# Optimization experiments

Hardware: AMD Instinct MI355X
Metric: run time of the kernel (lower is better)

Reference implementation:

```python
import jax, jax.numpy as jnp
import numpy as np

N_ITERS = 5
STRICT_MAXIMA_BONUS = 10.0
MAX_SUBPIXEL_SHIFT = 0.6
DILATION_RADIUS = 1
EPS = 1e-7


def _dense_solve(x):
    """Per-voxel 3x3x3 quadratic-fit solve (Cramer's rule) on interior voxels.

    Returns full-size (zero-padded) sx, sy, ss, g.s, solved arrays.
    Axis convention: s = depth/scale (D), y = height (H), x = width (W).
    """
    c  = x[:, :, 1:-1, 1:-1, 1:-1]
    xp = x[:, :, 1:-1, 1:-1, 2:];   xm = x[:, :, 1:-1, 1:-1, :-2]
    yp = x[:, :, 1:-1, 2:, 1:-1];   ym = x[:, :, 1:-1, :-2, 1:-1]
    sp = x[:, :, 2:, 1:-1, 1:-1];   sm = x[:, :, :-2, 1:-1, 1:-1]
    xpyp = x[:, :, 1:-1, 2:, 2:];   xmyp = x[:, :, 1:-1, 2:, :-2]
    xpym = x[:, :, 1:-1, :-2, 2:];  xmym = x[:, :, 1:-1, :-2, :-2]
    xpsp = x[:, :, 2:, 1:-1, 2:];   xmsp = x[:, :, 2:, 1:-1, :-2]
    xpsm = x[:, :, :-2, 1:-1, 2:];  xmsm = x[:, :, :-2, 1:-1, :-2]
    ypsp = x[:, :, 2:, 2:, 1:-1];   ymsp = x[:, :, 2:, :-2, 1:-1]
    ypsm = x[:, :, :-2, 2:, 1:-1];  ymsm = x[:, :, :-2, :-2, 1:-1]
    gx = 0.5 * (xp - xm)
    gy = 0.5 * (yp - ym)
    gs = 0.5 * (sp - sm)
    dxx = xp - 2.0 * c + xm
    dyy = yp - 2.0 * c + ym
    dss = sp - 2.0 * c + sm
    dxy = 0.25 * (xpyp - xmyp - xpym + xmym)
    dxs = 0.25 * (xpsp - xmsp - xpsm + xmsm)
    dys = 0.25 * (ypsp - ymsp - ypsm + ymsm)
    cf00 = dyy * dss - dys * dys
    cf01 = dxy * dss - dys * dxs
    cf02 = dxy * dys - dyy * dxs
    det = dxx * cf00 - dxy * cf01 + dxs * cf02
    solved = jnp.abs(det) > EPS
    safe_det = jnp.where(solved, det, jnp.ones_like(det))
    r0, r1, r2 = -gx, -gy, -gs
    sx = (r0 * cf00 - dxy * (r1 * dss - dys * r2) + dxs * (r1 * dys - dyy * r2)) / safe_det
    sy = (dxx * (r1 * dss - dys * r2) - r0 * cf01 + dxs * (dxy * r2 - r1 * dxs)) / safe_det
    ss = (dxx * (dyy * r2 - r1 * dys) - dxy * (dxy * r2 - r1 * dxs) + r0 * cf02) / safe_det
    gds = gx * sx + gy * sy + gs * ss
    pad = ((0, 0), (0, 0), (1, 1), (1, 1), (1, 1))
    return (jnp.pad(sx, pad), jnp.pad(sy, pad), jnp.pad(ss, pad),
            jnp.pad(gds, pad), jnp.pad(solved, pad))


def reference(input, nms_mask):
    x = input
    B, C, D, H, W = x.shape
    dt = x.dtype
    HW = H * W
    DHW = D * HW
    r = DILATION_RADIUS

    sx_f, sy_f, ss_f, gds_f, sol_f = _dense_solve(x)
    sx_f = sx_f.reshape(-1); sy_f = sy_f.reshape(-1); ss_f = ss_f.reshape(-1)
    gds_f = gds_f.reshape(-1); sol_f = sol_f.reshape(-1)
    xf = x.reshape(-1)

    dg = jnp.arange(D, dtype=jnp.int32)[:, None, None]
    hg = jnp.arange(H, dtype=jnp.int32)[None, :, None]
    wg = jnp.arange(W, dtype=jnp.int32)[None, None, :]
    bcg = (jnp.arange(B * C, dtype=jnp.int32) * DHW).reshape(B, C, 1, 1, 1)

    zi = jnp.zeros((B, C, D, H, W), jnp.int32)
    dd, dh, dw = zi, zi, zi              # integer centre offsets (s, y, x)
    valid = nms_mask                      # only NMS maxima are tracked
    zf = jnp.zeros((B, C, D, H, W), dt)
    shift_x, shift_y, shift_s, gds_k = zf, zf, zf, zf

    for _ in range(N_ITERS):
        di = jnp.clip(dg + dd, 1, D - 2)
        hi = jnp.clip(hg + dh, 1, H - 2)
        wi = jnp.clip(wg + dw, 1, W - 2)
        flat = bcg + di * HW + hi * W + wi
        sx = sx_f[flat]; sy = sy_f[flat]; ss = ss_f[flat]
        gds = gds_f[flat]; sol = sol_f[flat]
        valid = valid & sol
        vf = valid.astype(dt)
        shift_x = sx * vf
        shift_y = sy * vf
        shift_s = ss * vf
        gds_k = gds * vf
        step_x = (jnp.sign(shift_x) * (jnp.abs(shift_x) > MAX_SUBPIXEL_SHIFT)).astype(jnp.int32)
        step_y = (jnp.sign(shift_y) * (jnp.abs(shift_y) > MAX_SUBPIXEL_SHIFT)).astype(jnp.int32)
        step_s = (jnp.sign(shift_s) * (jnp.abs(shift_s) > MAX_SUBPIXEL_SHIFT)).astype(jnp.int32)
        dw = dw + step_x; dh = dh + step_y; dd = dd + step_s
        # moving outside the dilated precompute region invalidates the keypoint
        valid = valid & (jnp.abs(dd) <= r) & (jnp.abs(dh) <= r) & (jnp.abs(dw) <= r)

    di = jnp.clip(dg + dd, 1, D - 2)
    hi = jnp.clip(hg + dh, 1, H - 2)
    wi = jnp.clip(wg + dw, 1, W - 2)
    flat = bcg + di * HW + hi * W + wi
    cur_val = xf[flat]

    refined = jnp.where(valid, cur_val + 0.5 * gds_k, x)
    y_max = jnp.where(nms_mask, refined + STRICT_MAXIMA_BONUS, x)

    fd = dg.astype(dt); fh = hg.astype(dt); fw = wg.astype(dt)
    cs = jnp.where(valid, (dg + dd).astype(dt) + shift_s, jnp.broadcast_to(fd, x.shape))
    cx = jnp.where(valid, (wg + dw).astype(dt) + shift_x, jnp.broadcast_to(fw, x.shape))
    cy = jnp.where(valid, (hg + dh).astype(dt) + shift_y, jnp.broadcast_to(fh, x.shape))
    coords_max = jnp.stack([cs, cx, cy], axis=2)  # (B,C,3,D,H,W): [scale, x, y]
    return coords_max, y_max


def setup_inputs() -> dict:
    key = jax.random.key(0)
    k1, k2 = jax.random.split(key)
    B, C, D, H, W = 2, 4, 6, 512, 512
    x = jax.random.normal(k1, (B, C, D, H, W), dtype=jnp.float32)
    m = jax.random.uniform(k2, (B, C, D, H, W)) < 0.001
    interior = jnp.zeros((B, C, D, H, W), dtype=bool).at[:, :, 1:-1, 1:-1, 1:-1].set(True)
    return {"input": x, "nms_mask": m & interior}
```

## Files before the change

### kernel.cpp

```cpp
#include <hip/hip_runtime.h>

#pragma clang fp contract(off)

constexpr int B_ = 2, C_ = 4, D_ = 6, H_ = 512, W_ = 512;
constexpr int HW_  = H_ * W_;
constexpr int DHW_ = D_ * HW_;
constexpr int BC_  = B_ * C_;
constexpr int TOT_ = BC_ * DHW_;

#define EPS_ 1e-7f
#define MAX_SHIFT_ 0.6f
#define BONUS_ 10.0f
#define N_ITERS_ 5

typedef float f32x4 __attribute__((ext_vector_type(4)));
typedef int   i32x4 __attribute__((ext_vector_type(4)));

__device__ __forceinline__ void solve3(const float* __restrict__ p,
                                       float& sx, float& sy, float& ss,
                                       float& gds, bool& sol)
{
    #pragma clang fp contract(off)
    float c    = p[0];
    float xp   = p[1],          xm   = p[-1];
    float yp   = p[W_],         ym   = p[-W_];
    float spv  = p[HW_],        smv  = p[-HW_];
    float xpyp = p[W_ + 1],     xmyp = p[W_ - 1];
    float xpym = p[-W_ + 1],    xmym = p[-W_ - 1];
    float xpsp = p[HW_ + 1],    xmsp = p[HW_ - 1];
    float xpsm = p[-HW_ + 1],   xmsm = p[-HW_ - 1];
    float ypsp = p[HW_ + W_],   ymsp = p[HW_ - W_];
    float ypsm = p[-HW_ + W_],  ymsm = p[-HW_ - W_];

    float gx = 0.5f * (xp - xm);
    float gy = 0.5f * (yp - ym);
    float gs = 0.5f * (spv - smv);
    float dxx = xp - 2.0f * c + xm;
    float dyy = yp - 2.0f * c + ym;
    float dss = spv - 2.0f * c + smv;
    float dxy = 0.25f * (xpyp - xmyp - xpym + xmym);
    float dxs = 0.25f * (xpsp - xmsp - xpsm + xmsm);
    float dys = 0.25f * (ypsp - ymsp - ypsm + ymsm);

    float cf00 = dyy * dss - dys * dys;
    float cf01 = dxy * dss - dys * dxs;
    float cf02 = dxy * dys - dyy * dxs;
    float det  = dxx * cf00 - dxy * cf01 + dxs * cf02;
    sol = fabsf(det) > EPS_;
    float sd = sol ? det : 1.0f;
    float r0 = -gx, r1 = -gy, r2 = -gs;
    sx = (r0 * cf00 - dxy * (r1 * dss - dys * r2) + dxs * (r1 * dys - dyy * r2)) / sd;
    sy = (dxx * (r1 * dss - dys * r2) - r0 * cf01 + dxs * (dxy * r2 - r1 * dxs)) / sd;
    ss = (dxx * (dyy * r2 - r1 * dys) - dxy * (dxy * r2 - r1 * dxs) + r0 * cf02) / sd;
    gds = gx * sx + gy * sy + gs * ss;
}

__global__ __launch_bounds__(256)
void AdaptiveQuadInterp3d_kernel(const float* __restrict__ x,
                                 const int* __restrict__ mask,
                                 float* __restrict__ out)
{
    int tid = blockIdx.x * 256 + threadIdx.x;
    int e   = tid * 4;

    int w0 = e & (W_ - 1);
    int h  = (e >> 9) & (H_ - 1);
    int t  = e >> 18;
    int d  = t % D_;
    int bc = t / D_;
    int sp = e - bc * DHW_;

    const f32x4 xv = *reinterpret_cast<const f32x4*>(x + e);
    const i32x4 mv = *reinterpret_cast<const i32x4*>(mask + e);

    float fd = (float)d, fh = (float)h;
    float cs0 = fd, cs1 = fd, cs2 = fd, cs3 = fd;
    float cx0 = (float)w0,       cx1 = (float)(w0 + 1);
    float cx2 = (float)(w0 + 2), cx3 = (float)(w0 + 3);
    float cy0 = fh, cy1 = fh, cy2 = fh, cy3 = fh;
    float y0 = xv.x, y1 = xv.y, y2 = xv.z, y3 = xv.w;

    int anym = mv.x | mv.y | mv.z | mv.w;

    if (__ballot(anym != 0) != 0ULL) {
        if (anym != 0) {
            const float* xb = x + bc * DHW_;

            auto walk = [&](int mj, int w, float xc,
                            float& cs, float& cx, float& cy, float& yy) {
                #pragma clang fp contract(off)
                if (mj == 0) return;
                int dsd = 0, dsh = 0, dsw = 0;
                bool valid = true;
                float shx = 0.0f, shy = 0.0f, shs = 0.0f, gk = 0.0f;

                #pragma unroll 1
                for (int it = 0; it < N_ITERS_; ++it) {
                    int di = min(max(d + dsd, 1), D_ - 2);
                    int hi = min(max(h + dsh, 1), H_ - 2);
                    int wi = min(max(w + dsw, 1), W_ - 2);
                    const float* p = xb + di * HW_ + hi * W_ + wi;

                    float sx, sy, ssv, gds; bool sol;
                    solve3(p, sx, sy, ssv, gds, sol);

                    if (!sol) { valid = false; break; }

                    shx = sx; shy = sy; shs = ssv; gk = gds;

                    int stx = (shx > MAX_SHIFT_) ? 1 : ((shx < -MAX_SHIFT_) ? -1 : 0);
                    int sty = (shy > MAX_SHIFT_) ? 1 : ((shy < -MAX_SHIFT_) ? -1 : 0);
                    int sts = (shs > MAX_SHIFT_) ? 1 : ((shs < -MAX_SHIFT_) ? -1 : 0);
                    dsw += stx;
                    dsh += sty;
                    dsd += sts;
                    valid = (abs(dsd) <= 1) && (abs(dsh) <= 1) && (abs(dsw) <= 1);
                    if (!valid) break;
                    if ((stx | sty | sts) == 0) break;
                }

                if (valid) {
                    int di = min(max(d + dsd, 1), D_ - 2);
                    int hi = min(max(h + dsh, 1), H_ - 2);
                    int wi = min(max(w + dsw, 1), W_ - 2);
                    float cur = xb[di * HW_ + hi * W_ + wi];
                    cs = (float)(d + dsd) + shs;
                    cx = (float)(w + dsw) + shx;
                    cy = (float)(h + dsh) + shy;
                    yy = (cur + 0.5f * gk) + BONUS_;
                } else {
                    yy = xc + BONUS_;
                }
            };

            walk(mv.x, w0 + 0, xv.x, cs0, cx0, cy0, y0);
            walk(mv.y, w0 + 1, xv.y, cs1, cx1, cy1, y1);
            walk(mv.z, w0 + 2, xv.z, cs2, cx2, cy2, y2);
            walk(mv.w, w0 + 3, xv.w, cs3, cx3, cy3, y3);
        }
    }

    f32x4 csv = { cs0, cs1, cs2, cs3 };
    f32x4 cxv = { cx0, cx1, cx2, cx3 };
    f32x4 cyv = { cy0, cy1, cy2, cy3 };
    f32x4 yv  = { y0,  y1,  y2,  y3  };

    float* cb = out + (bc * 3) * DHW_ + sp;
    __builtin_nontemporal_store(csv, reinterpret_cast<f32x4*>(cb));
    __builtin_nontemporal_store(cxv, reinterpret_cast<f32x4*>(cb + DHW_));
    __builtin_nontemporal_store(cyv, reinterpret_cast<f32x4*>(cb + 2 * DHW_));
    __builtin_nontemporal_store(yv,
        reinterpret_cast<f32x4*>(out + BC_ * 3 * DHW_ + e));
}

extern "C" void kernel_launch(void* const* d_in, const int* in_sizes, int n_in,
                              void* d_out, int out_size, void* d_ws, size_t ws_size,
                              hipStream_t stream) {
    const float* x    = (const float*)d_in[0];
    const int*   mask = (const int*)d_in[1];
    float*       out  = (float*)d_out;

    int blocks = TOT_ / (256 * 4);
    AdaptiveQuadInterp3d_kernel<<<blocks, 256, 0, stream>>>(x, mask, out);
}
```

Before: 275.0 us.

## Process eight elements per thread and store defaults before sparse refinement

```diff
diff --git a/kernel.cpp b/kernel.cpp
--- a/kernel.cpp
+++ b/kernel.cpp
@@ -61,7 +61,7 @@
                                  float* __restrict__ out)
 {
     int tid = blockIdx.x * 256 + threadIdx.x;
-    int e   = tid * 4;
+    int e   = tid * 8;
 
     int w0 = e & (W_ - 1);
     int h  = (e >> 9) & (H_ - 1);
@@ -70,26 +70,41 @@
     int bc = t / D_;
     int sp = e - bc * DHW_;
 
-    const f32x4 xv = *reinterpret_cast<const f32x4*>(x + e);
-    const i32x4 mv = *reinterpret_cast<const i32x4*>(mask + e);
+    const f32x4 xa = *reinterpret_cast<const f32x4*>(x + e);
+    const f32x4 xbv = *reinterpret_cast<const f32x4*>(x + e + 4);
+    const i32x4 ma = *reinterpret_cast<const i32x4*>(mask + e);
+    const i32x4 mb = *reinterpret_cast<const i32x4*>(mask + e + 4);
 
     float fd = (float)d, fh = (float)h;
-    float cs0 = fd, cs1 = fd, cs2 = fd, cs3 = fd;
-    float cx0 = (float)w0,       cx1 = (float)(w0 + 1);
-    float cx2 = (float)(w0 + 2), cx3 = (float)(w0 + 3);
-    float cy0 = fh, cy1 = fh, cy2 = fh, cy3 = fh;
-    float y0 = xv.x, y1 = xv.y, y2 = xv.z, y3 = xv.w;
+    float* cb = out + (bc * 3) * DHW_ + sp;
+    float* yb = out + BC_ * 3 * DHW_ + e;
 
-    int anym = mv.x | mv.y | mv.z | mv.w;
+    f32x4 csv = { fd, fd, fd, fd };
+    f32x4 cxa = { (float)w0,       (float)(w0 + 1),
+                  (float)(w0 + 2), (float)(w0 + 3) };
+    f32x4 cxb = { (float)(w0 + 4), (float)(w0 + 5),
+                  (float)(w0 + 6), (float)(w0 + 7) };
+    f32x4 cyv = { fh, fh, fh, fh };
+
+    __builtin_nontemporal_store(csv, reinterpret_cast<f32x4*>(cb));
+    __builtin_nontemporal_store(csv, reinterpret_cast<f32x4*>(cb + 4));
+    __builtin_nontemporal_store(cxa, reinterpret_cast<f32x4*>(cb + DHW_));
+    __builtin_nontemporal_store(cxb, reinterpret_cast<f32x4*>(cb + DHW_ + 4));
+    __builtin_nontemporal_store(cyv, reinterpret_cast<f32x4*>(cb + 2 * DHW_));
+    __builtin_nontemporal_store(cyv, reinterpret_cast<f32x4*>(cb + 2 * DHW_ + 4));
+    __builtin_nontemporal_store(xa,  reinterpret_cast<f32x4*>(yb));
+    __builtin_nontemporal_store(xbv, reinterpret_cast<f32x4*>(yb + 4));
+
+    int anym = ma.x | ma.y | ma.z | ma.w | mb.x | mb.y | mb.z | mb.w;
 
     if (__ballot(anym != 0) != 0ULL) {
         if (anym != 0) {
-            const float* xb = x + bc * DHW_;
+            const float* xbase = x + bc * DHW_;
 
-            auto walk = [&](int mj, int w, float xc,
-                            float& cs, float& cx, float& cy, float& yy) {
+            auto walk = [&](int mj, int j, float xc) {
                 #pragma clang fp contract(off)
                 if (mj == 0) return;
+                int w = w0 + j;
                 int dsd = 0, dsh = 0, dsw = 0;
                 bool valid = true;
                 float shx = 0.0f, shy = 0.0f, shs = 0.0f, gk = 0.0f;
@@ -99,7 +114,7 @@
                     int di = min(max(d + dsd, 1), D_ - 2);
                     int hi = min(max(h + dsh, 1), H_ - 2);
                     int wi = min(max(w + dsw, 1), W_ - 2);
-                    const float* p = xb + di * HW_ + hi * W_ + wi;
+                    const float* p = xbase + di * HW_ + hi * W_ + wi;
 
                     float sx, sy, ssv, gds; bool sol;
                     solve3(p, sx, sy, ssv, gds, sol);
@@ -123,34 +138,26 @@
                     int di = min(max(d + dsd, 1), D_ - 2);
                     int hi = min(max(h + dsh, 1), H_ - 2);
                     int wi = min(max(w + dsw, 1), W_ - 2);
-                    float cur = xb[di * HW_ + hi * W_ + wi];
-                    cs = (float)(d + dsd) + shs;
-                    cx = (float)(w + dsw) + shx;
-                    cy = (float)(h + dsh) + shy;
-                    yy = (cur + 0.5f * gk) + BONUS_;
+                    float cur = xbase[di * HW_ + hi * W_ + wi];
+                    __builtin_nontemporal_store((float)(d + dsd) + shs, cb + j);
+                    __builtin_nontemporal_store((float)(w + dsw) + shx, cb + DHW_ + j);
+                    __builtin_nontemporal_store((float)(h + dsh) + shy, cb + 2 * DHW_ + j);
+                    __builtin_nontemporal_store((cur + 0.5f * gk) + BONUS_, yb + j);
                 } else {
-                    yy = xc + BONUS_;
+                    __builtin_nontemporal_store(xc + BONUS_, yb + j);
                 }
             };
 
-            walk(mv.x, w0 + 0, xv.x, cs0, cx0, cy0, y0);
-            walk(mv.y, w0 + 1, xv.y, cs1, cx1, cy1, y1);
-            walk(mv.z, w0 + 2, xv.z, cs2, cx2, cy2, y2);
-            walk(mv.w, w0 + 3, xv.w, cs3, cx3, cy3, y3);
+            walk(ma.x, 0, xa.x);
+            walk(ma.y, 1, xa.y);
+            walk(ma.z, 2, xa.z);
+            walk(ma.w, 3, xa.w);
+            walk(mb.x, 4, xbv.x);
+            walk(mb.y, 5, xbv.y);
+            walk(mb.z, 6, xbv.z);
+            walk(mb.w, 7, xbv.w);
         }
     }
-
-    f32x4 csv = { cs0, cs1, cs2, cs3 };
-    f32x4 cxv = { cx0, cx1, cx2, cx3 };
-    f32x4 cyv = { cy0, cy1, cy2, cy3 };
-    f32x4 yv  = { y0,  y1,  y2,  y3  };
-
-    float* cb = out + (bc * 3) * DHW_ + sp;
-    __builtin_nontemporal_store(csv, reinterpret_cast<f32x4*>(cb));
-    __builtin_nontemporal_store(cxv, reinterpret_cast<f32x4*>(cb + DHW_));
-    __builtin_nontemporal_store(cyv, reinterpret_cast<f32x4*>(cb + 2 * DHW_));
-    __builtin_nontemporal_store(yv,
-        reinterpret_cast<f32x4*>(out + BC_ * 3 * DHW_ + e));
 }
 
 extern "C" void kernel_launch(void* const* d_in, const int* in_sizes, int n_in,
@@ -160,6 +167,6 @@
     const int*   mask = (const int*)d_in[1];
     float*       out  = (float*)d_out;
 
-    int blocks = TOT_ / (256 * 4);
+    int blocks = TOT_ / (256 * 8);
     AdaptiveQuadInterp3d_kernel<<<blocks, 256, 0, stream>>>(x, mask, out);
 }
```

After: 292.7 us. 1.06x slower.
